# Optimization experiments

Measured on AMD Instinct MI355X. Metric: run time of the kernel, lower is better.

The kernel has to match this reference:

```python
import jax, jax.numpy as jnp
import numpy as np

N_NODES = 50000
N_EDGES = 800000
IN_CH = 96
HID = 128
OUT_CH = 2


def _glorot(key, shape):
    lim = 1.0 / np.sqrt(shape[0])
    return jax.random.uniform(key, shape, jnp.float32, -lim, lim)


def setup_inputs() -> dict:
    key = jax.random.key(0)
    ks = jax.random.split(key, 16)
    x = jax.random.normal(ks[0], (N_NODES, IN_CH), jnp.float32)
    edge_index = jax.random.randint(ks[1], (2, N_EDGES), 0, N_NODES, jnp.int64)
    dims = [(IN_CH, HID), (HID, HID), (HID, HID // 2)]
    params = {}
    for i, (di, do) in enumerate(dims, start=1):
        params[f"Wl{i}"] = _glorot(ks[2 * i], (di, do))      # neighbor (lin_l)
        params[f"Wr{i}"] = _glorot(ks[2 * i + 1], (di, do))  # root (lin_r)
        params[f"b{i}"] = jnp.zeros((do,), jnp.float32)
    params["Wc"] = _glorot(ks[10], (HID // 2, OUT_CH))
    params["bc"] = jnp.zeros((OUT_CH,), jnp.float32)
    return {"x": x, "edge_index": edge_index, **params}


def _sage_conv(x, src, dst, Wl, Wr, b):
    # scatter-mean of source-node features into destination nodes (PyG mean aggr)
    n = x.shape[0]
    agg = jax.ops.segment_sum(x[src], dst, num_segments=n)          # [N, d]
    cnt = jax.ops.segment_sum(jnp.ones((src.shape[0], 1), x.dtype), dst, num_segments=n)
    mean = agg / jnp.maximum(cnt, 1.0)
    return mean @ Wl + x @ Wr + b


def reference(x, edge_index, Wl1, Wr1, b1, Wl2, Wr2, b2, Wl3, Wr3, b3, Wc, bc):
    src, dst = edge_index[0], edge_index[1]
    h = jax.nn.relu(_sage_conv(x, src, dst, Wl1, Wr1, b1))
    h = jax.nn.relu(_sage_conv(h, src, dst, Wl2, Wr2, b2))
    h = jax.nn.relu(_sage_conv(h, src, dst, Wl3, Wr3, b3))
    return h @ Wc + bc  # [N, 2] logits (dropout is identity at inference)
```

## Files before the change

kernel.cpp:

```cpp
#include <hip/hip_runtime.h>

#define N_NODES 50000
#define N_EDGES 800000
#define SCAN_NB ((N_NODES + 255) / 256)

#define NB_E 128
#define CH (N_EDGES / NB_E)
#define RSZ 25000
#define HALF_WORDS (RSZ / 2)

#define CVT_ITEMS  (N_NODES * 96 / 4)
#define CVT_NB  ((CVT_ITEMS + 255) / 256)
#define PACK1_NB 12
#define PACK2_NB 16
#define PACK3_NB 8
#define PREP_NB (CVT_NB + PACK1_NB + PACK2_NB + PACK3_NB)

typedef __attribute__((ext_vector_type(8))) short short8;
typedef __attribute__((ext_vector_type(8))) unsigned short ushort8;
typedef __attribute__((ext_vector_type(4))) float f32x4;

__device__ __forceinline__ float bf2f(unsigned short u) {
  unsigned int x = ((unsigned int)u) << 16;
  return __builtin_bit_cast(float, x);
}
__device__ __forceinline__ unsigned short f2bf(float f) {
  unsigned int x = __builtin_bit_cast(unsigned int, f);
  unsigned int r = x + 0x7FFFu + ((x >> 16) & 1u);
  return (unsigned short)(r >> 16);
}


__device__ __forceinline__ void pack_w_section(const float* __restrict__ Wl,
                                               const float* __restrict__ Wr,
                                               ushort* __restrict__ wcat,
                                               int K, int J2, int bid) {
  int idx = bid * 256 + threadIdx.x;
  int Jcat = 2 * J2;
  int total = (K / 8) * Jcat;
  if (idx >= total) return;
  int kk8 = idx / Jcat, j = idx % Jcat;
  const float* W = (j < J2) ? Wl : Wr;
  int jj = (j < J2) ? j : j - J2;
  ushort8 v;
  #pragma unroll
  for (int i = 0; i < 8; i++) v[i] = f2bf(W[(kk8 * 8 + i) * J2 + jj]);
  *(ushort8*)(wcat + (size_t)idx * 8) = v;
}

__global__ __launch_bounds__(256) void prep_kernel(
    const float* __restrict__ x, ushort* __restrict__ xb,
    const float* __restrict__ Wl1, const float* __restrict__ Wr1, ushort* __restrict__ wcat1,
    const float* __restrict__ Wl2, const float* __restrict__ Wr2, ushort* __restrict__ wcat2,
    const float* __restrict__ Wl3, const float* __restrict__ Wr3, ushort* __restrict__ wcat3) {
  int bid = blockIdx.x;
  if (bid < CVT_NB) {
    int i = bid * 256 + threadIdx.x;
    if (i < CVT_ITEMS) {
      f32x4 v = __builtin_nontemporal_load((const f32x4*)(x + i * 4));
      ushort4 o = make_ushort4(f2bf(v.x), f2bf(v.y), f2bf(v.z), f2bf(v.w));
      *(ushort4*)(xb + i * 4) = o;
    }
    return;
  }
  bid -= CVT_NB;
  if (bid < PACK1_NB) { pack_w_section(Wl1, Wr1, wcat1, 96, 128, bid); return; }
  bid -= PACK1_NB;
  if (bid < PACK2_NB) { pack_w_section(Wl2, Wr2, wcat2, 128, 128, bid); return; }
  bid -= PACK2_NB;
  pack_w_section(Wl3, Wr3, wcat3, 128, 64, bid);
}


__global__ __launch_bounds__(256) void hist_lds(const int* __restrict__ dst,
                                                ushort* __restrict__ hist_g) {
  __shared__ unsigned hist[HALF_WORDS];
  for (int j = threadIdx.x; j < HALF_WORDS; j += 256) hist[j] = 0;
  __syncthreads();
  int b = blockIdx.x >> 1, r = blockIdx.x & 1;
  int base = b * CH;
  for (int i = threadIdx.x; i < CH; i += 256) {
    int d = __builtin_nontemporal_load(dst + base + i);
    unsigned ld = (unsigned)(d - r * RSZ);
    if (ld < RSZ) atomicAdd(&hist[ld >> 1], (ld & 1) ? 65536u : 1u);
  }
  __syncthreads();
  unsigned* outp = (unsigned*)(hist_g + (size_t)b * N_NODES + r * RSZ);
  for (int j = threadIdx.x; j < HALF_WORDS; j += 256) outp[j] = hist[j];
}

__device__ __forceinline__ int block_excl_scan_256(int v, int tid, int* tot_out) {
  __shared__ int ws[4];
  int lane = tid & 63, wid = tid >> 6;
  int incl = v;
  #pragma unroll
  for (int off = 1; off < 64; off <<= 1) {
    int t = __shfl_up(incl, off);
    if (lane >= off) incl += t;
  }
  if (lane == 63) ws[wid] = incl;
  __syncthreads();
  int woff = 0;
  #pragma unroll
  for (int w = 0; w < 4; w++) woff += (w < wid) ? ws[w] : 0;
  *tot_out = ws[0] + ws[1] + ws[2] + ws[3];
  return woff + incl - v;
}

__global__ __launch_bounds__(256) void scanA(const ushort* __restrict__ hist_g,
                                             ushort* __restrict__ cum_g,
                                             int* __restrict__ rowptr,
                                             int* __restrict__ blocksum, int n) {
  int i = blockIdx.x * 256 + threadIdx.x;
  int run = 0;
  if (i < n) {
    for (int b = 0; b < NB_E; b++) {
      size_t o = (size_t)b * N_NODES + i;
      int c = hist_g[o];
      cum_g[o] = (ushort)run;
      run += c;
    }
  }
  int tot;
  int excl = block_excl_scan_256(run, threadIdx.x, &tot);
  if (i < n) rowptr[i] = excl;
  if (threadIdx.x == 0) blocksum[blockIdx.x] = tot;
}

__global__ __launch_bounds__(256) void scanB(const int* __restrict__ blocksum,
                                             int* __restrict__ blockoff,
                                             int* __restrict__ rowptr, int nb, int n) {
  int tid = threadIdx.x;
  int v = (tid < nb) ? blocksum[tid] : 0;
  int tot;
  int excl = block_excl_scan_256(v, tid, &tot);
  if (tid < nb) blockoff[tid] = excl;
  if (tid == 0) rowptr[n] = tot;
}

__global__ __launch_bounds__(256) void scanC(int* __restrict__ rowptr,
                                             const int* __restrict__ blockoff, int n) {
  int i = blockIdx.x * 256 + threadIdx.x;
  if (i < n) rowptr[i] += blockoff[blockIdx.x];
}

__global__ __launch_bounds__(256) void fill_lds(const int* __restrict__ src,
                                                const int* __restrict__ dst,
                                                const ushort* __restrict__ cum_g,
                                                const int* __restrict__ rowptr,
                                                ushort* __restrict__ csr) {
  __shared__ unsigned cur[HALF_WORDS];
  int b = blockIdx.x >> 1, r = blockIdx.x & 1;
  const unsigned* cg = (const unsigned*)(cum_g + (size_t)b * N_NODES + r * RSZ);
  for (int j = threadIdx.x; j < HALF_WORDS; j += 256) cur[j] = cg[j];
  __syncthreads();
  int base = b * CH;
  for (int i = threadIdx.x; i < CH; i += 256) {
    int d = __builtin_nontemporal_load(dst + base + i);
    int s = __builtin_nontemporal_load(src + base + i);
    unsigned ld = (unsigned)(d - r * RSZ);
    if (ld < RSZ) {
      unsigned old = atomicAdd(&cur[ld >> 1], (ld & 1) ? 65536u : 1u);
      unsigned loc = (ld & 1) ? (old >> 16) : (old & 0xffffu);
      csr[(size_t)rowptr[d] + loc] = (ushort)s;
    }
  }
}

template <int K, int J2>
__global__ __launch_bounds__(256) void gemm_mfma(
    const ushort* __restrict__ hb, const ushort* __restrict__ wcat,
    ushort* __restrict__ tl, ushort* __restrict__ tr, int n) {
  constexpr int Jcat = 2 * J2;
  constexpr int NT = Jcat / 16;
  constexpr int KS = K / 32;
  constexpr int BM = 128;
  constexpr int LDS_US = (BM * Jcat > K * Jcat) ? BM * Jcat : K * Jcat;
  __shared__ ushort lds[LDS_US];

  int tid = threadIdx.x;
  int wid = tid >> 6, lane = tid & 63;
  int row0 = blockIdx.x * BM;

  constexpr int WCH = K * Jcat / 8;
  for (int c = tid; c < WCH; c += 256) {
    *(ushort8*)(lds + c * 8) = *(const ushort8*)(wcat + (size_t)c * 8);
  }
  __syncthreads();

  int rg = lane >> 4, lc = lane & 15;
  int r0 = row0 + wid * 32 + lc;
  int r1 = r0 + 16;
  long ar0 = (long)min(r0, n - 1) * K;
  long ar1 = (long)min(r1, n - 1) * K;

  f32x4 acc[2][NT];
  #pragma unroll
  for (int mt = 0; mt < 2; mt++)
    #pragma unroll
    for (int jt = 0; jt < NT; jt++) acc[mt][jt] = (f32x4){0.f, 0.f, 0.f, 0.f};

  #pragma unroll
  for (int ks = 0; ks < KS; ks++) {
    int koff = ks * 32 + rg * 8;
    short8 a0 = *(const short8*)(hb + ar0 + koff);
    short8 a1 = *(const short8*)(hb + ar1 + koff);
    int kk8 = ks * 4 + rg;
    #pragma unroll
    for (int jt = 0; jt < NT; jt++) {
      short8 bfr = *(const short8*)(lds + ((size_t)kk8 * Jcat + jt * 16 + lc) * 8);
      acc[0][jt] = __builtin_amdgcn_mfma_f32_16x16x32_bf16(a0, bfr, acc[0][jt], 0, 0, 0);
      acc[1][jt] = __builtin_amdgcn_mfma_f32_16x16x32_bf16(a1, bfr, acc[1][jt], 0, 0, 0);
    }
  }
  __syncthreads();

  #pragma unroll
  for (int mt = 0; mt < 2; mt++) {
    int rbase = wid * 32 + mt * 16 + rg * 4;
    #pragma unroll
    for (int jt = 0; jt < NT; jt++) {
      int col = jt * 16 + lc;
      #pragma unroll
      for (int r = 0; r < 4; r++)
        lds[(size_t)(rbase + r) * Jcat + col] = f2bf(acc[mt][jt][r]);
    }
  }
  __syncthreads();

  constexpr int CPR = J2 / 8;
  for (int i = tid; i < BM * 2 * CPR; i += 256) {
    int row = i / (2 * CPR), cc = i % (2 * CPR);
    int grow = row0 + row;
    if (grow < n) {
      ushort8 v = *(ushort8*)(lds + (size_t)row * Jcat + cc * 8);
      ushort* dstp = (cc < CPR) ? (tl + (size_t)grow * J2 + cc * 8)
                                : (tr + (size_t)grow * J2 + (size_t)(cc - CPR) * 8);
      *(ushort8*)dstp = v;
    }
  }
}

__global__ __launch_bounds__(256) void agg_relu128(
    const ushort* __restrict__ tl, const ushort* __restrict__ tr,
    const float* __restrict__ bias,
    const int* __restrict__ rowptr, const ushort* __restrict__ csr,
    ushort* __restrict__ hout, int n) {
  int node = blockIdx.x * 16 + (threadIdx.x >> 4);
  int lane = threadIdx.x & 15;
  if (node >= n) return;
  int lo = rowptr[node], hi = rowptr[node + 1];

  float s[8];
  #pragma unroll
  for (int i = 0; i < 8; i++) s[i] = 0.f;

  int e = lo;
  for (; e + 1 < hi; e += 2) {
    int i0 = csr[e], i1 = csr[e + 1];
    ushort8 v0 = *(const ushort8*)(tl + (size_t)i0 * 128 + lane * 8);
    ushort8 v1 = *(const ushort8*)(tl + (size_t)i1 * 128 + lane * 8);
    #pragma unroll
    for (int i = 0; i < 8; i++) s[i] += bf2f(v0[i]) + bf2f(v1[i]);
  }
  if (e < hi) {
    int i0 = csr[e];
    ushort8 v0 = *(const ushort8*)(tl + (size_t)i0 * 128 + lane * 8);
    #pragma unroll
    for (int i = 0; i < 8; i++) s[i] += bf2f(v0[i]);
  }

  int deg = hi - lo;
  float inv = (deg > 0) ? 1.f / (float)deg : 0.f;
  ushort8 tv = *(const ushort8*)(tr + (size_t)node * 128 + lane * 8);
  float4 b0 = *(const float4*)(bias + lane * 8);
  float4 b1 = *(const float4*)(bias + lane * 8 + 4);
  float bb[8] = {b0.x, b0.y, b0.z, b0.w, b1.x, b1.y, b1.z, b1.w};
  ushort8 o;
  #pragma unroll
  for (int i = 0; i < 8; i++) {
    float v = s[i] * inv + bf2f(tv[i]) + bb[i];
    o[i] = f2bf(v > 0.f ? v : 0.f);
  }
  *(ushort8*)(hout + (size_t)node * 128 + lane * 8) = o;
}

__global__ __launch_bounds__(256) void agg_head(
    const ushort* __restrict__ tl, const ushort* __restrict__ tr,
    const float* __restrict__ bias, const float* __restrict__ Wc,
    const float* __restrict__ bc,
    const int* __restrict__ rowptr, const ushort* __restrict__ csr,
    float* __restrict__ out, int n) {
  int node = blockIdx.x * 32 + (threadIdx.x >> 3);
  int lane = threadIdx.x & 7;
  if (node >= n) return;
  int lo = rowptr[node], hi = rowptr[node + 1];

  float s[8];
  #pragma unroll
  for (int i = 0; i < 8; i++) s[i] = 0.f;

  int e = lo;
  for (; e + 1 < hi; e += 2) {
    int i0 = csr[e], i1 = csr[e + 1];
    ushort8 v0 = *(const ushort8*)(tl + (size_t)i0 * 64 + lane * 8);
    ushort8 v1 = *(const ushort8*)(tl + (size_t)i1 * 64 + lane * 8);
    #pragma unroll
    for (int i = 0; i < 8; i++) s[i] += bf2f(v0[i]) + bf2f(v1[i]);
  }
  if (e < hi) {
    int i0 = csr[e];
    ushort8 v0 = *(const ushort8*)(tl + (size_t)i0 * 64 + lane * 8);
    #pragma unroll
    for (int i = 0; i < 8; i++) s[i] += bf2f(v0[i]);
  }

  int deg = hi - lo;
  float inv = (deg > 0) ? 1.f / (float)deg : 0.f;
  ushort8 tv = *(const ushort8*)(tr + (size_t)node * 64 + lane * 8);
  float p0 = 0.f, p1 = 0.f;
  #pragma unroll
  for (int i = 0; i < 8; i++) {
    int k = lane * 8 + i;
    float v = s[i] * inv + bf2f(tv[i]) + bias[k];
    v = v > 0.f ? v : 0.f;
    p0 += v * Wc[k * 2 + 0];
    p1 += v * Wc[k * 2 + 1];
  }
  #pragma unroll
  for (int off = 1; off < 8; off <<= 1) {
    p0 += __shfl_xor(p0, off);
    p1 += __shfl_xor(p1, off);
  }
  if (lane == 0) {
    out[(size_t)node * 2 + 0] = p0 + bc[0];
    out[(size_t)node * 2 + 1] = p1 + bc[1];
  }
}

extern "C" void kernel_launch(void* const* d_in, const int* in_sizes, int n_in,
                              void* d_out, int out_size, void* d_ws, size_t ws_size,
                              hipStream_t stream) {
  const float* x   = (const float*)d_in[0];
  const int*   ei  = (const int*)d_in[1];
  const float* Wl1 = (const float*)d_in[2];
  const float* Wr1 = (const float*)d_in[3];
  const float* b1  = (const float*)d_in[4];
  const float* Wl2 = (const float*)d_in[5];
  const float* Wr2 = (const float*)d_in[6];
  const float* b2  = (const float*)d_in[7];
  const float* Wl3 = (const float*)d_in[8];
  const float* Wr3 = (const float*)d_in[9];
  const float* b3  = (const float*)d_in[10];
  const float* Wc  = (const float*)d_in[11];
  const float* bc  = (const float*)d_in[12];
  float* out = (float*)d_out;

  const int* src = ei;
  const int* dst = ei + N_EDGES;

  char* ws = (char*)d_ws;
  size_t off = 0;
  auto alloc = [&](size_t bytes) -> void* {
    void* p = ws + off;
    off += (bytes + 255) & ~(size_t)255;
    return p;
  };
  int*    rowptr   = (int*)alloc((N_NODES + 1) * sizeof(int));
  ushort* csr      = (ushort*)alloc(N_EDGES * sizeof(ushort));
  int*    blocksum = (int*)alloc(256 * sizeof(int));
  int*    blockoff = (int*)alloc(256 * sizeof(int));
  ushort* xb       = (ushort*)alloc((size_t)N_NODES * 96 * 2);
  ushort* wcat1    = (ushort*)alloc((size_t)96 * 256 * 2);
  ushort* wcat2    = (ushort*)alloc((size_t)128 * 256 * 2);
  ushort* wcat3    = (ushort*)alloc((size_t)128 * 128 * 2);
  ushort* tl       = (ushort*)alloc((size_t)N_NODES * 128 * 2);
  ushort* tr       = (ushort*)alloc((size_t)N_NODES * 128 * 2);
  ushort* hA       = (ushort*)alloc((size_t)N_NODES * 128 * 2);
  ushort* hB       = (ushort*)alloc((size_t)N_NODES * 128 * 2);
  (void)ws_size; (void)n_in; (void)in_sizes; (void)out_size;

  ushort* hist_g = tl;
  ushort* cum_g  = tr;

  prep_kernel<<<PREP_NB, 256, 0, stream>>>(x, xb,
                                           Wl1, Wr1, wcat1,
                                           Wl2, Wr2, wcat2,
                                           Wl3, Wr3, wcat3);

  hist_lds<<<NB_E * 2, 256, 0, stream>>>(dst, hist_g);
  scanA<<<SCAN_NB, 256, 0, stream>>>(hist_g, cum_g, rowptr, blocksum, N_NODES);
  scanB<<<1, 256, 0, stream>>>(blocksum, blockoff, rowptr, SCAN_NB, N_NODES);
  scanC<<<SCAN_NB, 256, 0, stream>>>(rowptr, blockoff, N_NODES);
  fill_lds<<<NB_E * 2, 256, 0, stream>>>(src, dst, cum_g, rowptr, csr);

  const int gemm_grid = (N_NODES + 127) / 128;
  const int agg_grid  = (N_NODES + 15) / 16;
  const int head_grid = (N_NODES + 31) / 32;

  gemm_mfma<96, 128><<<gemm_grid, 256, 0, stream>>>(xb, wcat1, tl, tr, N_NODES);
  agg_relu128<<<agg_grid, 256, 0, stream>>>(tl, tr, b1, rowptr, csr, hA, N_NODES);
  gemm_mfma<128, 128><<<gemm_grid, 256, 0, stream>>>(hA, wcat2, tl, tr, N_NODES);
  agg_relu128<<<agg_grid, 256, 0, stream>>>(tl, tr, b2, rowptr, csr, hB, N_NODES);
  gemm_mfma<128, 64><<<gemm_grid, 256, 0, stream>>>(hB, wcat3, tl, tr, N_NODES);
  agg_head<<<head_grid, 256, 0, stream>>>(tl, tr, b3, Wc, bc, rowptr, csr, out, N_NODES);
}
```

Before: 195.3 us.

## Fuse neighbor aggregation with following layer GEMM via LDS staging

Replaces the separate agg_relu128 and gemm_mfma launches for layers 2 and 3 with a single kernel. Each block aggregates 128 nodes into an LDS tile, applies mean, bias and ReLU, then runs the MFMA GEMM for the next layer directly from LDS. This removes the global round trip of the hidden activations and two launches. It also unrolls the edge gather loops by four for more loads in flight. In exchange, the gather phase uses fewer threads per node per block, and the output stores become scalar per-element writes instead of LDS-staged vector writes.

New measurement: 226.9 us. 16.2% more time.

```diff
diff --git a/kernel.cpp b/kernel.cpp
--- a/kernel.cpp
+++ b/kernel.cpp
@@ -241,48 +241,110 @@
   }
 }
 
-__global__ __launch_bounds__(256) void agg_relu128(
-    const ushort* __restrict__ tl, const ushort* __restrict__ tr,
+template <int J2out>
+__global__ __launch_bounds__(256) void fused_agg_gemm(
+    const ushort* __restrict__ tlin, const ushort* __restrict__ trin,
     const float* __restrict__ bias,
     const int* __restrict__ rowptr, const ushort* __restrict__ csr,
-    ushort* __restrict__ hout, int n) {
-  int node = blockIdx.x * 16 + (threadIdx.x >> 4);
-  int lane = threadIdx.x & 15;
-  if (node >= n) return;
-  int lo = rowptr[node], hi = rowptr[node + 1];
-
-  float s[8];
-  #pragma unroll
-  for (int i = 0; i < 8; i++) s[i] = 0.f;
-
-  int e = lo;
-  for (; e + 1 < hi; e += 2) {
-    int i0 = csr[e], i1 = csr[e + 1];
-    ushort8 v0 = *(const ushort8*)(tl + (size_t)i0 * 128 + lane * 8);
-    ushort8 v1 = *(const ushort8*)(tl + (size_t)i1 * 128 + lane * 8);
-    #pragma unroll
-    for (int i = 0; i < 8; i++) s[i] += bf2f(v0[i]) + bf2f(v1[i]);
-  }
-  if (e < hi) {
-    int i0 = csr[e];
-    ushort8 v0 = *(const ushort8*)(tl + (size_t)i0 * 128 + lane * 8);
-    #pragma unroll
-    for (int i = 0; i < 8; i++) s[i] += bf2f(v0[i]);
-  }
-
-  int deg = hi - lo;
-  float inv = (deg > 0) ? 1.f / (float)deg : 0.f;
-  ushort8 tv = *(const ushort8*)(tr + (size_t)node * 128 + lane * 8);
-  float4 b0 = *(const float4*)(bias + lane * 8);
-  float4 b1 = *(const float4*)(bias + lane * 8 + 4);
-  float bb[8] = {b0.x, b0.y, b0.z, b0.w, b1.x, b1.y, b1.z, b1.w};
-  ushort8 o;
-  #pragma unroll
-  for (int i = 0; i < 8; i++) {
-    float v = s[i] * inv + bf2f(tv[i]) + bb[i];
-    o[i] = f2bf(v > 0.f ? v : 0.f);
-  }
-  *(ushort8*)(hout + (size_t)node * 128 + lane * 8) = o;
+    const ushort* __restrict__ wcat,
+    ushort* __restrict__ tlout, ushort* __restrict__ trout, int n) {
+  constexpr int K = 128;
+  constexpr int Jcat = 2 * J2out;
+  constexpr int NT = Jcat / 16;
+  constexpr int KS = K / 32;
+  constexpr int HP = K + 8;
+  __shared__ ushort h[128 * HP];
+
+  int tid = threadIdx.x;
+  int row0 = blockIdx.x * 128;
+
+  {
+    int lane16 = tid & 15;
+    int ngrp = tid >> 4;
+    float4 b0 = *(const float4*)(bias + lane16 * 8);
+    float4 b1 = *(const float4*)(bias + lane16 * 8 + 4);
+    float bb[8] = {b0.x, b0.y, b0.z, b0.w, b1.x, b1.y, b1.z, b1.w};
+    for (int p = 0; p < 8; p++) {
+      int ng = p * 16 + ngrp;
+      int node = row0 + ng;
+      ushort8 o;
+      if (node < n) {
+        int lo = rowptr[node], hi = rowptr[node + 1];
+        float s[8];
+        #pragma unroll
+        for (int i = 0; i < 8; i++) s[i] = 0.f;
+        int e = lo;
+        for (; e + 3 < hi; e += 4) {
+          int i0 = csr[e], i1 = csr[e + 1], i2 = csr[e + 2], i3 = csr[e + 3];
+          ushort8 v0 = *(const ushort8*)(tlin + (size_t)i0 * 128 + lane16 * 8);
+          ushort8 v1 = *(const ushort8*)(tlin + (size_t)i1 * 128 + lane16 * 8);
+          ushort8 v2 = *(const ushort8*)(tlin + (size_t)i2 * 128 + lane16 * 8);
+          ushort8 v3 = *(const ushort8*)(tlin + (size_t)i3 * 128 + lane16 * 8);
+          #pragma unroll
+          for (int i = 0; i < 8; i++)
+            s[i] += (bf2f(v0[i]) + bf2f(v1[i])) + (bf2f(v2[i]) + bf2f(v3[i]));
+        }
+        for (; e < hi; e++) {
+          int i0 = csr[e];
+          ushort8 v0 = *(const ushort8*)(tlin + (size_t)i0 * 128 + lane16 * 8);
+          #pragma unroll
+          for (int i = 0; i < 8; i++) s[i] += bf2f(v0[i]);
+        }
+        int deg = hi - lo;
+        float inv = (deg > 0) ? 1.f / (float)deg : 0.f;
+        ushort8 tv = *(const ushort8*)(trin + (size_t)node * 128 + lane16 * 8);
+        #pragma unroll
+        for (int i = 0; i < 8; i++) {
+          float v = s[i] * inv + bf2f(tv[i]) + bb[i];
+          o[i] = f2bf(v > 0.f ? v : 0.f);
+        }
+      } else {
+        #pragma unroll
+        for (int i = 0; i < 8; i++) o[i] = 0;
+      }
+      *(ushort8*)(h + (size_t)ng * HP + lane16 * 8) = o;
+    }
+  }
+  __syncthreads();
+
+  int wid = tid >> 6, lane = tid & 63;
+  int rg = lane >> 4, lc = lane & 15;
+
+  f32x4 acc[2][NT];
+  #pragma unroll
+  for (int mt = 0; mt < 2; mt++)
+    #pragma unroll
+    for (int jt = 0; jt < NT; jt++) acc[mt][jt] = (f32x4){0.f, 0.f, 0.f, 0.f};
+
+  #pragma unroll
+  for (int ks = 0; ks < KS; ks++) {
+    int koff = ks * 32 + rg * 8;
+    short8 a0 = *(const short8*)(h + (size_t)(wid * 32 + lc) * HP + koff);
+    short8 a1 = *(const short8*)(h + (size_t)(wid * 32 + 16 + lc) * HP + koff);
+    int kk8 = ks * 4 + rg;
+    #pragma unroll
+    for (int jt = 0; jt < NT; jt++) {
+      short8 bfr = *(const short8*)(wcat + ((size_t)kk8 * Jcat + jt * 16 + lc) * 8);
+      acc[0][jt] = __builtin_amdgcn_mfma_f32_16x16x32_bf16(a0, bfr, acc[0][jt], 0, 0, 0);
+      acc[1][jt] = __builtin_amdgcn_mfma_f32_16x16x32_bf16(a1, bfr, acc[1][jt], 0, 0, 0);
+    }
+  }
+
+  #pragma unroll
+  for (int mt = 0; mt < 2; mt++) {
+    int rbase = wid * 32 + mt * 16 + rg * 4;
+    #pragma unroll
+    for (int jt = 0; jt < NT; jt++) {
+      int col = jt * 16 + lc;
+      ushort* outp = (col < J2out) ? tlout : trout;
+      int cm = (col < J2out) ? col : col - J2out;
+      #pragma unroll
+      for (int r = 0; r < 4; r++) {
+        int grow = row0 + rbase + r;
+        if (grow < n) outp[(size_t)grow * J2out + cm] = f2bf(acc[mt][jt][r]);
+      }
+    }
+  }
 }
 
 __global__ __launch_bounds__(256) void agg_head(
@@ -301,14 +363,17 @@
   for (int i = 0; i < 8; i++) s[i] = 0.f;
 
   int e = lo;
-  for (; e + 1 < hi; e += 2) {
-    int i0 = csr[e], i1 = csr[e + 1];
+  for (; e + 3 < hi; e += 4) {
+    int i0 = csr[e], i1 = csr[e + 1], i2 = csr[e + 2], i3 = csr[e + 3];
     ushort8 v0 = *(const ushort8*)(tl + (size_t)i0 * 64 + lane * 8);
     ushort8 v1 = *(const ushort8*)(tl + (size_t)i1 * 64 + lane * 8);
-    #pragma unroll
-    for (int i = 0; i < 8; i++) s[i] += bf2f(v0[i]) + bf2f(v1[i]);
-  }
-  if (e < hi) {
+    ushort8 v2 = *(const ushort8*)(tl + (size_t)i2 * 64 + lane * 8);
+    ushort8 v3 = *(const ushort8*)(tl + (size_t)i3 * 64 + lane * 8);
+    #pragma unroll
+    for (int i = 0; i < 8; i++)
+      s[i] += (bf2f(v0[i]) + bf2f(v1[i])) + (bf2f(v2[i]) + bf2f(v3[i]));
+  }
+  for (; e < hi; e++) {
     int i0 = csr[e];
     ushort8 v0 = *(const ushort8*)(tl + (size_t)i0 * 64 + lane * 8);
     #pragma unroll
@@ -394,14 +459,13 @@
   scanC<<<SCAN_NB, 256, 0, stream>>>(rowptr, blockoff, N_NODES);
   fill_lds<<<NB_E * 2, 256, 0, stream>>>(src, dst, cum_g, rowptr, csr);
 
-  const int gemm_grid = (N_NODES + 127) / 128;
-  const int agg_grid  = (N_NODES + 15) / 16;
-  const int head_grid = (N_NODES + 31) / 32;
-
-  gemm_mfma<96, 128><<<gemm_grid, 256, 0, stream>>>(xb, wcat1, tl, tr, N_NODES);
-  agg_relu128<<<agg_grid, 256, 0, stream>>>(tl, tr, b1, rowptr, csr, hA, N_NODES);
-  gemm_mfma<128, 128><<<gemm_grid, 256, 0, stream>>>(hA, wcat2, tl, tr, N_NODES);
-  agg_relu128<<<agg_grid, 256, 0, stream>>>(tl, tr, b2, rowptr, csr, hB, N_NODES);
-  gemm_mfma<128, 64><<<gemm_grid, 256, 0, stream>>>(hB, wcat3, tl, tr, N_NODES);
-  agg_head<<<head_grid, 256, 0, stream>>>(tl, tr, b3, Wc, bc, rowptr, csr, out, N_NODES);
-}
+  const int ngrid = (N_NODES + 127) / 128;
+
+  gemm_mfma<96, 128><<<ngrid, 256, 0, stream>>>(xb, wcat1, tl, tr, N_NODES);
+  fused_agg_gemm<128><<<ngrid, 256, 0, stream>>>(tl, tr, b1, rowptr, csr, wcat2,
+                                                 hA, hB, N_NODES);
+  fused_agg_gemm<64><<<ngrid, 256, 0, stream>>>(hA, hB, b2, rowptr, csr, wcat3,
+                                                tl, tr, N_NODES);
+  agg_head<<<(N_NODES + 31) / 32, 256, 0, stream>>>(tl, tr, b3, Wc, bc,
+                                                    rowptr, csr, out, N_NODES);
+}
```

## Split 128-wide neighbor aggregation into four 32-column passes with deeper unrolling

Applied to the files above, without the earlier changes.

The 128-channel mean aggregation now runs as four launches, each gathering a 32-column slice of the transformed features. The per-pass working set (50000 nodes x 64 bytes) is small enough to stay in L2/MALL across random gathers. Edge loops are unrolled by four, and CSR index loads use nontemporal hints in both the 128-wide and head kernels. In exchange the CSR indices and rowptr are read four times and there are extra kernel launches, and each gather is now only 16 bytes per lane.

Result: slower. 266.1 us (+36.3%).

```diff
diff --git a/kernel.cpp b/kernel.cpp
--- a/kernel.cpp
+++ b/kernel.cpp
@@ -241,40 +241,48 @@
   }
 }
 
-__global__ __launch_bounds__(256) void agg_relu128(
-    const ushort* __restrict__ tl, const ushort* __restrict__ tr,
+__global__ __launch_bounds__(256) void agg_pass128(
+    const ushort* __restrict__ tlin, const ushort* __restrict__ trin,
     const float* __restrict__ bias,
     const int* __restrict__ rowptr, const ushort* __restrict__ csr,
-    ushort* __restrict__ hout, int n) {
-  int node = blockIdx.x * 16 + (threadIdx.x >> 4);
-  int lane = threadIdx.x & 15;
+    ushort* __restrict__ hout, int c0, int n) {
+  int node = blockIdx.x * 64 + (threadIdx.x >> 2);
+  int lane = threadIdx.x & 3;
   if (node >= n) return;
+  int col = c0 + lane * 8;
   int lo = rowptr[node], hi = rowptr[node + 1];
+  const ushort* tb = tlin + col;
 
   float s[8];
   #pragma unroll
   for (int i = 0; i < 8; i++) s[i] = 0.f;
 
   int e = lo;
-  for (; e + 1 < hi; e += 2) {
-    int i0 = csr[e], i1 = csr[e + 1];
-    ushort8 v0 = *(const ushort8*)(tl + (size_t)i0 * 128 + lane * 8);
-    ushort8 v1 = *(const ushort8*)(tl + (size_t)i1 * 128 + lane * 8);
-    #pragma unroll
-    for (int i = 0; i < 8; i++) s[i] += bf2f(v0[i]) + bf2f(v1[i]);
-  }
-  if (e < hi) {
-    int i0 = csr[e];
-    ushort8 v0 = *(const ushort8*)(tl + (size_t)i0 * 128 + lane * 8);
+  for (; e + 3 < hi; e += 4) {
+    int i0 = __builtin_nontemporal_load(csr + e);
+    int i1 = __builtin_nontemporal_load(csr + e + 1);
+    int i2 = __builtin_nontemporal_load(csr + e + 2);
+    int i3 = __builtin_nontemporal_load(csr + e + 3);
+    ushort8 v0 = *(const ushort8*)(tb + (size_t)i0 * 128);
+    ushort8 v1 = *(const ushort8*)(tb + (size_t)i1 * 128);
+    ushort8 v2 = *(const ushort8*)(tb + (size_t)i2 * 128);
+    ushort8 v3 = *(const ushort8*)(tb + (size_t)i3 * 128);
+    #pragma unroll
+    for (int i = 0; i < 8; i++)
+      s[i] += (bf2f(v0[i]) + bf2f(v1[i])) + (bf2f(v2[i]) + bf2f(v3[i]));
+  }
+  for (; e < hi; e++) {
+    int i0 = __builtin_nontemporal_load(csr + e);
+    ushort8 v0 = *(const ushort8*)(tb + (size_t)i0 * 128);
     #pragma unroll
     for (int i = 0; i < 8; i++) s[i] += bf2f(v0[i]);
   }
 
   int deg = hi - lo;
   float inv = (deg > 0) ? 1.f / (float)deg : 0.f;
-  ushort8 tv = *(const ushort8*)(tr + (size_t)node * 128 + lane * 8);
-  float4 b0 = *(const float4*)(bias + lane * 8);
-  float4 b1 = *(const float4*)(bias + lane * 8 + 4);
+  ushort8 tv = __builtin_nontemporal_load((const ushort8*)(trin + (size_t)node * 128 + col));
+  float4 b0 = *(const float4*)(bias + col);
+  float4 b1 = *(const float4*)(bias + col + 4);
   float bb[8] = {b0.x, b0.y, b0.z, b0.w, b1.x, b1.y, b1.z, b1.w};
   ushort8 o;
   #pragma unroll
@@ -282,7 +290,7 @@
     float v = s[i] * inv + bf2f(tv[i]) + bb[i];
     o[i] = f2bf(v > 0.f ? v : 0.f);
   }
-  *(ushort8*)(hout + (size_t)node * 128 + lane * 8) = o;
+  *(ushort8*)(hout + (size_t)node * 128 + col) = o;
 }
 
 __global__ __launch_bounds__(256) void agg_head(
@@ -301,15 +309,21 @@
   for (int i = 0; i < 8; i++) s[i] = 0.f;
 
   int e = lo;
-  for (; e + 1 < hi; e += 2) {
-    int i0 = csr[e], i1 = csr[e + 1];
+  for (; e + 3 < hi; e += 4) {
+    int i0 = __builtin_nontemporal_load(csr + e);
+    int i1 = __builtin_nontemporal_load(csr + e + 1);
+    int i2 = __builtin_nontemporal_load(csr + e + 2);
+    int i3 = __builtin_nontemporal_load(csr + e + 3);
     ushort8 v0 = *(const ushort8*)(tl + (size_t)i0 * 64 + lane * 8);
     ushort8 v1 = *(const ushort8*)(tl + (size_t)i1 * 64 + lane * 8);
-    #pragma unroll
-    for (int i = 0; i < 8; i++) s[i] += bf2f(v0[i]) + bf2f(v1[i]);
-  }
-  if (e < hi) {
-    int i0 = csr[e];
+    ushort8 v2 = *(const ushort8*)(tl + (size_t)i2 * 64 + lane * 8);
+    ushort8 v3 = *(const ushort8*)(tl + (size_t)i3 * 64 + lane * 8);
+    #pragma unroll
+    for (int i = 0; i < 8; i++)
+      s[i] += (bf2f(v0[i]) + bf2f(v1[i])) + (bf2f(v2[i]) + bf2f(v3[i]));
+  }
+  for (; e < hi; e++) {
+    int i0 = __builtin_nontemporal_load(csr + e);
     ushort8 v0 = *(const ushort8*)(tl + (size_t)i0 * 64 + lane * 8);
     #pragma unroll
     for (int i = 0; i < 8; i++) s[i] += bf2f(v0[i]);
@@ -395,13 +409,15 @@
   fill_lds<<<NB_E * 2, 256, 0, stream>>>(src, dst, cum_g, rowptr, csr);
 
   const int gemm_grid = (N_NODES + 127) / 128;
-  const int agg_grid  = (N_NODES + 15) / 16;
+  const int agg_grid  = (N_NODES + 63) / 64;
   const int head_grid = (N_NODES + 31) / 32;
 
   gemm_mfma<96, 128><<<gemm_grid, 256, 0, stream>>>(xb, wcat1, tl, tr, N_NODES);
-  agg_relu128<<<agg_grid, 256, 0, stream>>>(tl, tr, b1, rowptr, csr, hA, N_NODES);
+  for (int c0 = 0; c0 < 128; c0 += 32)
+    agg_pass128<<<agg_grid, 256, 0, stream>>>(tl, tr, b1, rowptr, csr, hA, c0, N_NODES);
   gemm_mfma<128, 128><<<gemm_grid, 256, 0, stream>>>(hA, wcat2, tl, tr, N_NODES);
-  agg_relu128<<<agg_grid, 256, 0, stream>>>(tl, tr, b2, rowptr, csr, hB, N_NODES);
+  for (int c0 = 0; c0 < 128; c0 += 32)
+    agg_pass128<<<agg_grid, 256, 0, stream>>>(tl, tr, b2, rowptr, csr, hB, c0, N_NODES);
   gemm_mfma<128, 64><<<gemm_grid, 256, 0, stream>>>(hB, wcat3, tl, tr, N_NODES);
   agg_head<<<head_grid, 256, 0, stream>>>(tl, tr, b3, Wc, bc, rowptr, csr, out, N_NODES);
 }
```
